# Kernel tuning notes

Measured on AMD Instinct MI355X. Metric: run time of the kernel, lower is better.

The kernel has to match this reference:

```python
import jax, jax.numpy as jnp
import numpy as np

K0 = 5.0
ISIZE = (1024.0, 1024.0)  # image (h, w) from ishape
POOL = (7, 7)


def crop_and_resize(feat, boxes, pool):
    """TF tf.image.crop_and_resize (bilinear, extrapolation_value=0) for a single
    image. feat: [H, W, C]; boxes: [N, 4] normalized [y1, x1, y2, x2].
    Returns [N, ph, pw, C]."""
    H, W, C = feat.shape
    ph, pw = pool
    y1, x1, y2, x2 = boxes[:, 0], boxes[:, 1], boxes[:, 2], boxes[:, 3]
    dt = feat.dtype
    # sample grid (ph>1, pw>1 branch of TF kernel)
    iy = y1[:, None] * (H - 1) + jnp.arange(ph, dtype=dt)[None, :] * ((y2 - y1) * (H - 1) / (ph - 1))[:, None]  # [N, ph]
    ix = x1[:, None] * (W - 1) + jnp.arange(pw, dtype=dt)[None, :] * ((x2 - x1) * (W - 1) / (pw - 1))[:, None]  # [N, pw]
    y0f = jnp.floor(iy)
    x0f = jnp.floor(ix)
    ly = (iy - y0f)[:, :, None, None]
    lx = (ix - x0f)[:, None, :, None]
    y0 = jnp.clip(y0f.astype(jnp.int32), 0, H - 1)
    y1i = jnp.clip(y0f.astype(jnp.int32) + 1, 0, H - 1)
    x0 = jnp.clip(x0f.astype(jnp.int32), 0, W - 1)
    x1i = jnp.clip(x0f.astype(jnp.int32) + 1, 0, W - 1)
    f00 = feat[y0[:, :, None], x0[:, None, :]]   # [N, ph, pw, C]
    f01 = feat[y0[:, :, None], x1i[:, None, :]]
    f10 = feat[y1i[:, :, None], x0[:, None, :]]
    f11 = feat[y1i[:, :, None], x1i[:, None, :]]
    top = f00 + (f01 - f00) * lx
    bot = f10 + (f11 - f10) * lx
    val = top + (bot - top) * ly
    valid = (((iy >= 0) & (iy <= H - 1))[:, :, None, None]
             & ((ix >= 0) & (ix <= W - 1))[:, None, :, None])
    return jnp.where(valid, val, jnp.zeros((), dt))


def setup_inputs() -> dict:
    key = jax.random.key(0)
    kf0, kf1, kf2, kf3, kh, kw, ky, kx = jax.random.split(key, 8)
    C = 256
    feat0 = jax.random.normal(kf0, (1, 256, 256, C), dtype=jnp.float32)
    feat1 = jax.random.normal(kf1, (1, 128, 128, C), dtype=jnp.float32)
    feat2 = jax.random.normal(kf2, (1, 64, 64, C), dtype=jnp.float32)
    feat3 = jax.random.normal(kf3, (1, 32, 32, C), dtype=jnp.float32)
    N = 1000
    # box sizes log-uniform in [16, 512] px so levels 0..3 are all exercised
    h = 2.0 ** jax.random.uniform(kh, (N,), minval=4.0, maxval=9.0)
    w = 2.0 ** jax.random.uniform(kw, (N,), minval=4.0, maxval=9.0)
    y1 = jax.random.uniform(ky, (N,)) * (ISIZE[0] - h)
    x1 = jax.random.uniform(kx, (N,)) * (ISIZE[1] - w)
    rois = jnp.stack([y1, x1, y1 + h, x1 + w], axis=1)[None].astype(jnp.float32)  # [1, N, 4]
    return {"feat0": feat0, "feat1": feat1, "feat2": feat2, "feat3": feat3, "rois": rois}


def reference(feat0, feat1, feat2, feat3, rois):
    r = rois[0]  # [N, 4] = [y1, x1, y2, x2]
    h = r[:, 2] - r[:, 0]
    w = r[:, 3] - r[:, 1]
    lvl = jnp.log(jnp.sqrt(h * w)) / jnp.log(2.0)
    lvl = jnp.clip(jnp.round(lvl - K0).astype(jnp.int32), 0, 3)  # [N]
    scale = jnp.array([ISIZE[0], ISIZE[1], ISIZE[0], ISIZE[1]], dtype=r.dtype)
    norm = jax.lax.stop_gradient(r / scale)  # normbox2d + tf.stop_gradient
    # tf.where/gather_nd per level + concat == stable sort of rois by level
    order = jnp.argsort(lvl, stable=True)
    s_lvl = lvl[order]
    s_box = norm[order]
    feats = [feat0[0], feat1[0], feat2[0], feat3[0]]
    N = r.shape[0]
    out = jnp.zeros((N, POOL[0], POOL[1], feat0.shape[-1]), feat0.dtype)
    for l, f in enumerate(feats):  # fixed 4 FPN levels, structurally distinct shapes
        crops = crop_and_resize(f, s_box, POOL)
        out = jnp.where((s_lvl == l)[:, None, None, None], crops, out)
    return out[None]  # [1, N, ph, pw, C]
```

## Files before the change

### kernel.cpp

```cpp
#include <hip/hip_runtime.h>

#define POOL_H 7
#define POOL_W 7
#define CHANS  256

__global__ void __launch_bounds__(1024) level_sort_kernel(
    const float* __restrict__ rois, int N,
    int* __restrict__ sorted_lvl, float4* __restrict__ sorted_box)
{
    __shared__ int hist[16][4];

    const int tid  = threadIdx.x;
    const int wave = tid >> 6;
    const int lane = tid & 63;

    int lvl = -1;
    float y1 = 0.f, x1 = 0.f, y2 = 0.f, x2 = 0.f;
    if (tid < N) {
        y1 = rois[tid * 4 + 0];
        x1 = rois[tid * 4 + 1];
        y2 = rois[tid * 4 + 2];
        x2 = rois[tid * 4 + 3];
        float h = y2 - y1;
        float w = x2 - x1;
        float l = logf(sqrtf(h * w)) / logf(2.0f);
        int li = (int)rintf(l - 5.0f);
        lvl = li < 0 ? 0 : (li > 3 ? 3 : li);
    }

    unsigned long long mask[4];
    #pragma unroll
    for (int l = 0; l < 4; ++l) mask[l] = __ballot(lvl == l);
    if (lane == 0) {
        #pragma unroll
        for (int l = 0; l < 4; ++l) hist[wave][l] = __popcll(mask[l]);
    }
    __syncthreads();

    if (lvl >= 0) {
        int pos = __popcll(mask[lvl] & ((1ull << lane) - 1ull));
        for (int w2 = 0; w2 < wave; ++w2) pos += hist[w2][lvl];
        for (int l = 0; l < lvl; ++l)
            #pragma unroll
            for (int w2 = 0; w2 < 16; ++w2) pos += hist[w2][l];

        sorted_lvl[pos] = lvl;
        const float inv = 1.0f / 1024.0f;
        sorted_box[pos] = make_float4(y1 * inv, x1 * inv, y2 * inv, x2 * inv);
    }
}

__global__ void __launch_bounds__(256) roi_align_kernel(
    const float* __restrict__ f0, const float* __restrict__ f1,
    const float* __restrict__ f2, const float* __restrict__ f3,
    const int* __restrict__ sorted_lvl, const float4* __restrict__ sorted_box,
    float* __restrict__ out)
{
    const int n    = blockIdx.x;
    const int wave = threadIdx.x >> 6;
    const int lane = threadIdx.x & 63;

    const int p = blockIdx.y * 4 + wave;
    if (p >= POOL_H * POOL_W) return;

    const int lvl = sorted_lvl[n];
    const float4 box = sorted_box[n];

    const float* feat;
    int HW;
    switch (lvl) {
        case 0:  feat = f0; HW = 256; break;
        case 1:  feat = f1; HW = 128; break;
        case 2:  feat = f2; HW = 64;  break;
        default: feat = f3; HW = 32;  break;
    }
    const float Hm1 = (float)(HW - 1);

    const int py = p / POOL_W;
    const int px = p % POOL_W;

    const float iy = box.x * Hm1 + (float)py * ((box.z - box.x) * Hm1 * (1.0f / 6.0f));
    const float ix = box.y * Hm1 + (float)px * ((box.w - box.y) * Hm1 * (1.0f / 6.0f));

    const float y0f = floorf(iy);
    const float x0f = floorf(ix);
    const float ly = iy - y0f;
    const float lx = ix - x0f;

    int y0  = (int)y0f;
    int x0  = (int)x0f;
    int y1i = y0 + 1;
    int x1i = x0 + 1;
    y0  = min(max(y0, 0), HW - 1);
    y1i = min(max(y1i, 0), HW - 1);
    x0  = min(max(x0, 0), HW - 1);
    x1i = min(max(x1i, 0), HW - 1);

    const bool valid = (iy >= 0.0f) & (iy <= Hm1) & (ix >= 0.0f) & (ix <= Hm1);

    const float4* p00 = (const float4*)(feat + ((size_t)(y0  * HW + x0 )) * CHANS) + lane;
    const float4* p01 = (const float4*)(feat + ((size_t)(y0  * HW + x1i)) * CHANS) + lane;
    const float4* p10 = (const float4*)(feat + ((size_t)(y1i * HW + x0 )) * CHANS) + lane;
    const float4* p11 = (const float4*)(feat + ((size_t)(y1i * HW + x1i)) * CHANS) + lane;

    const float4 f00 = *p00;
    const float4 f01 = *p01;
    const float4 f10 = *p10;
    const float4 f11 = *p11;

    float4 val;
    {
        float tx, bx;
        tx = f00.x + (f01.x - f00.x) * lx;
        bx = f10.x + (f11.x - f10.x) * lx;
        val.x = tx + (bx - tx) * ly;
        tx = f00.y + (f01.y - f00.y) * lx;
        bx = f10.y + (f11.y - f10.y) * lx;
        val.y = tx + (bx - tx) * ly;
        tx = f00.z + (f01.z - f00.z) * lx;
        bx = f10.z + (f11.z - f10.z) * lx;
        val.z = tx + (bx - tx) * ly;
        tx = f00.w + (f01.w - f00.w) * lx;
        bx = f10.w + (f11.w - f10.w) * lx;
        val.w = tx + (bx - tx) * ly;
    }
    if (!valid) { val.x = 0.f; val.y = 0.f; val.z = 0.f; val.w = 0.f; }

    float4* outn = (float4*)(out + (size_t)n * (POOL_H * POOL_W * CHANS));
    outn[p * 64 + lane] = val;
}

extern "C" void kernel_launch(void* const* d_in, const int* in_sizes, int n_in,
                              void* d_out, int out_size, void* d_ws, size_t ws_size,
                              hipStream_t stream) {
    const float* f0   = (const float*)d_in[0];
    const float* f1   = (const float*)d_in[1];
    const float* f2   = (const float*)d_in[2];
    const float* f3   = (const float*)d_in[3];
    const float* rois = (const float*)d_in[4];
    const int N = in_sizes[4] / 4;

    int*    sorted_lvl = (int*)d_ws;
    float4* sorted_box = (float4*)((char*)d_ws + 4096);
    float*  out        = (float*)d_out;

    hipLaunchKernelGGL(level_sort_kernel, dim3(1), dim3(1024), 0, stream,
                       rois, N, sorted_lvl, sorted_box);

    const int npos_blocks = (POOL_H * POOL_W + 3) / 4;
    hipLaunchKernelGGL(roi_align_kernel, dim3(N, npos_blocks), dim3(256), 0, stream,
                       f0, f1, f2, f3, sorted_lvl, sorted_box, out);
}
```

Before: 133.0 us.

## Process one ROI per block with a wave per pooled row and nontemporal stores

The roi_align launch changes from 13 blocks per ROI (4 pooled positions each) to one 448-thread block per ROI. Each of its 7 waves handles one pooled row and loops over the 7 columns, computing the y interpolation and row pointers once per row. Output writes use nontemporal stores so the large output stream does not pollute the cache. The cost is fewer, larger blocks with a serial column loop per wave, which may reduce memory-level parallelism per wave.

```diff
diff --git a/kernel.cpp b/kernel.cpp
--- a/kernel.cpp
+++ b/kernel.cpp
@@ -3,6 +3,8 @@
 #define POOL_H 7
 #define POOL_W 7
 #define CHANS  256
+
+typedef float v4f __attribute__((ext_vector_type(4)));
 
 __global__ void __launch_bounds__(1024) level_sort_kernel(
     const float* __restrict__ rois, int N,
@@ -50,18 +52,15 @@
     }
 }
 
-__global__ void __launch_bounds__(256) roi_align_kernel(
+__global__ void __launch_bounds__(448) roi_align_kernel(
     const float* __restrict__ f0, const float* __restrict__ f1,
     const float* __restrict__ f2, const float* __restrict__ f3,
     const int* __restrict__ sorted_lvl, const float4* __restrict__ sorted_box,
     float* __restrict__ out)
 {
     const int n    = blockIdx.x;
-    const int wave = threadIdx.x >> 6;
+    const int py   = threadIdx.x >> 6;
     const int lane = threadIdx.x & 63;
-
-    const int p = blockIdx.y * 4 + wave;
-    if (p >= POOL_H * POOL_W) return;
 
     const int lvl = sorted_lvl[n];
     const float4 box = sorted_box[n];
@@ -76,58 +75,64 @@
     }
     const float Hm1 = (float)(HW - 1);
 
-    const int py = p / POOL_W;
-    const int px = p % POOL_W;
+    const float sy = (box.z - box.x) * Hm1 * (1.0f / 6.0f);
+    const float sx = (box.w - box.y) * Hm1 * (1.0f / 6.0f);
 
-    const float iy = box.x * Hm1 + (float)py * ((box.z - box.x) * Hm1 * (1.0f / 6.0f));
-    const float ix = box.y * Hm1 + (float)px * ((box.w - box.y) * Hm1 * (1.0f / 6.0f));
+    const float iy  = box.x * Hm1 + (float)py * sy;
+    const float y0f = floorf(iy);
+    const float ly  = iy - y0f;
+    int y0  = (int)y0f;
+    int y1i = y0 + 1;
+    y0  = min(max(y0,  0), HW - 1);
+    y1i = min(max(y1i, 0), HW - 1);
+    const bool vy = (iy >= 0.0f) & (iy <= Hm1);
 
-    const float y0f = floorf(iy);
-    const float x0f = floorf(ix);
-    const float ly = iy - y0f;
-    const float lx = ix - x0f;
+    const float4* row0 = (const float4*)(feat + (size_t)(y0  * HW) * CHANS) + lane;
+    const float4* row1 = (const float4*)(feat + (size_t)(y1i * HW) * CHANS) + lane;
 
-    int y0  = (int)y0f;
-    int x0  = (int)x0f;
-    int y1i = y0 + 1;
-    int x1i = x0 + 1;
-    y0  = min(max(y0, 0), HW - 1);
-    y1i = min(max(y1i, 0), HW - 1);
-    x0  = min(max(x0, 0), HW - 1);
-    x1i = min(max(x1i, 0), HW - 1);
+    float4* outp = (float4*)(out + (size_t)n * (POOL_H * POOL_W * CHANS))
+                   + py * (POOL_W * 64) + lane;
 
-    const bool valid = (iy >= 0.0f) & (iy <= Hm1) & (ix >= 0.0f) & (ix <= Hm1);
+    const float ix_base = box.y * Hm1;
 
-    const float4* p00 = (const float4*)(feat + ((size_t)(y0  * HW + x0 )) * CHANS) + lane;
-    const float4* p01 = (const float4*)(feat + ((size_t)(y0  * HW + x1i)) * CHANS) + lane;
-    const float4* p10 = (const float4*)(feat + ((size_t)(y1i * HW + x0 )) * CHANS) + lane;
-    const float4* p11 = (const float4*)(feat + ((size_t)(y1i * HW + x1i)) * CHANS) + lane;
+    #pragma unroll
+    for (int px = 0; px < POOL_W; ++px) {
+        const float ix  = ix_base + (float)px * sx;
+        const float x0f = floorf(ix);
+        const float lx  = ix - x0f;
+        int x0  = (int)x0f;
+        int x1i = x0 + 1;
+        x0  = min(max(x0,  0), HW - 1);
+        x1i = min(max(x1i, 0), HW - 1);
+        const bool valid = vy & (ix >= 0.0f) & (ix <= Hm1);
 
-    const float4 f00 = *p00;
-    const float4 f01 = *p01;
-    const float4 f10 = *p10;
-    const float4 f11 = *p11;
+        const float4 f00 = row0[(size_t)x0  * 64];
+        const float4 f01 = row0[(size_t)x1i * 64];
+        const float4 f10 = row1[(size_t)x0  * 64];
+        const float4 f11 = row1[(size_t)x1i * 64];
 
-    float4 val;
-    {
-        float tx, bx;
-        tx = f00.x + (f01.x - f00.x) * lx;
-        bx = f10.x + (f11.x - f10.x) * lx;
-        val.x = tx + (bx - tx) * ly;
-        tx = f00.y + (f01.y - f00.y) * lx;
-        bx = f10.y + (f11.y - f10.y) * lx;
-        val.y = tx + (bx - tx) * ly;
-        tx = f00.z + (f01.z - f00.z) * lx;
-        bx = f10.z + (f11.z - f10.z) * lx;
-        val.z = tx + (bx - tx) * ly;
-        tx = f00.w + (f01.w - f00.w) * lx;
-        bx = f10.w + (f11.w - f10.w) * lx;
-        val.w = tx + (bx - tx) * ly;
+        float4 val;
+        {
+            float tx, bx;
+            tx = f00.x + (f01.x - f00.x) * lx;
+            bx = f10.x + (f11.x - f10.x) * lx;
+            val.x = tx + (bx - tx) * ly;
+            tx = f00.y + (f01.y - f00.y) * lx;
+            bx = f10.y + (f11.y - f10.y) * lx;
+            val.y = tx + (bx - tx) * ly;
+            tx = f00.z + (f01.z - f00.z) * lx;
+            bx = f10.z + (f11.z - f10.z) * lx;
+            val.z = tx + (bx - tx) * ly;
+            tx = f00.w + (f01.w - f00.w) * lx;
+            bx = f10.w + (f11.w - f10.w) * lx;
+            val.w = tx + (bx - tx) * ly;
+        }
+        if (!valid) { val.x = 0.f; val.y = 0.f; val.z = 0.f; val.w = 0.f; }
+
+        v4f vv;
+        vv.x = val.x; vv.y = val.y; vv.z = val.z; vv.w = val.w;
+        __builtin_nontemporal_store(vv, (v4f*)&outp[px * 64]);
     }
-    if (!valid) { val.x = 0.f; val.y = 0.f; val.z = 0.f; val.w = 0.f; }
-
-    float4* outn = (float4*)(out + (size_t)n * (POOL_H * POOL_W * CHANS));
-    outn[p * 64 + lane] = val;
 }
 
 extern "C" void kernel_launch(void* const* d_in, const int* in_sizes, int n_in,
@@ -147,7 +152,6 @@
     hipLaunchKernelGGL(level_sort_kernel, dim3(1), dim3(1024), 0, stream,
                        rois, N, sorted_lvl, sorted_box);
 
-    const int npos_blocks = (POOL_H * POOL_W + 3) / 4;
-    hipLaunchKernelGGL(roi_align_kernel, dim3(N, npos_blocks), dim3(256), 0, stream,
+    hipLaunchKernelGGL(roi_align_kernel, dim3(N), dim3(448), 0, stream,
                        f0, f1, f2, f3, sorted_lvl, sorted_box, out);
 }
```

Result: slower. 137.9 us (+3.6%).
